# Optimization experiments

Measured on AMD Instinct MI355X. Metric: run time of the kernel, lower is better.

The kernel has to match this reference:

```python
import jax, jax.numpy as jnp
import numpy as np
from jax import lax

# Matches init_kwargs: ops='co', window_size=[51, 25]
OPS = "co"
WINDOWS = [51, 25]


def _stage(x, k, mode):
    # Torch Conv1d(padding='same') zero-pads left=(k-1)//2, right=k//2, and the
    # identity-shift kernel bank + channel min/max is exactly a sliding-window
    # min/max over the zero-padded signal.
    left, right = (k - 1) // 2, k // 2
    xp = jnp.pad(x, ((0, 0), (0, 0), (left, right)))  # zeros, as in torch 'same'
    if mode == "max":  # dilation
        return lax.reduce_window(xp, float("-inf"), lax.max, (1, 1, k), (1, 1, 1), "VALID")
    # erosion
    return lax.reduce_window(xp, float("inf"), lax.min, (1, 1, k), (1, 1, 1), "VALID")


def _chain(x):
    # Per-channel python loop in the original is channel-independent; we batch it.
    for op, k in zip(OPS, WINDOWS):
        if op.lower() == "c":  # closing: dilation then erosion
            x = _stage(x, k, "max")
            x = _stage(x, k, "min")
        elif op.lower() == "o":  # opening: erosion then dilation
            x = _stage(x, k, "min")
            x = _stage(x, k, "max")
    return x


def setup_inputs() -> dict:
    key = jax.random.key(0)
    x = jax.random.normal(key, (16, 8, 262144), dtype=jnp.float32)  # [B, C, L]
    return {"x": x}


def reference(x):
    return _chain(x)
```

## Files before the change

### kernel.cpp

```cpp
#include <hip/hip_runtime.h>


#define L_ROW   262144
#define N_ROWS  128
#define BLOCK   64
#define E       32
#define EF4     8
#define T_W     1880
#define N_CHUNKS 140
#define NSLOT   512

typedef float f32x2 __attribute__((ext_vector_type(2)));

__device__ __forceinline__ int swz(int s) { return s ^ ((s >> 3) & 7); }

#define WFENCE() asm volatile("" ::: "memory")

template<bool MX>
__device__ __forceinline__ float mm(float a, float b) {
  return MX ? fmaxf(a, b) : fminf(a, b);
}

__device__ __forceinline__ void edge_zero(float* r, int goff, int lane, bool edge) {
  if (edge) {
    const int base = goff + lane * E;
#pragma unroll
    for (int i = 0; i < E; ++i)
      if ((unsigned)(base + i) >= (unsigned)L_ROW) r[i] = 0.0f;
  }
}

__device__ __forceinline__ void writeback(const float* r, float4* buf, int b4) {
  WFENCE();
#pragma unroll
  for (int j = 0; j < EF4; ++j)
    buf[swz(b4 + j)] = make_float4(r[4*j], r[4*j+1], r[4*j+2], r[4*j+3]);
  WFENCE();
}

template<int K, bool MX>
__device__ __forceinline__ void stage_big(float* r, float4* buf, int lane,
                                          int goff, bool edge) {
  constexpr int BLEN = K - 33;
  constexpr int BN   = (BLEN + 2) / 4;
  const int b4 = lane * EF4;
  const int bh = min(b4, NSLOT - 16 - BN);

  float4 v0 = buf[swz(bh + 8)];
  float a0 = v0.x, a1 = v0.y, a2 = v0.z, a3 = v0.w;
#pragma unroll
  for (int j = 1; j < BN - 1; ++j) {
    float4 v = buf[swz(bh + 8 + j)];
    a0 = mm<MX>(a0, v.x); a1 = mm<MX>(a1, v.y);
    a2 = mm<MX>(a2, v.z); a3 = mm<MX>(a3, v.w);
  }
  float4 vl = buf[swz(bh + 8 + BN - 1)];
  const float Base = mm<MX>(mm<MX>(mm<MX>(a0, a1), mm<MX>(a2, a3)),
                            mm<MX>(vl.x, vl.y));
  float T[34];
  T[0] = vl.z; T[1] = vl.w;
#pragma unroll
  for (int j = 0; j < 8; ++j) {
    float4 v = buf[swz(bh + 8 + BN + j)];
    T[2+4*j] = v.x; T[3+4*j] = v.y; T[4+4*j] = v.z; T[5+4*j] = v.w;
  }

#pragma unroll
  for (int b = 0; b < 4; ++b)
#pragma unroll
    for (int i = 8*b + 6; i >= 8*b; --i) r[i] = mm<MX>(r[i], r[i+1]);
  const float S2 = r[24];
  const float S1 = mm<MX>(r[16], S2);
  const float S0 = mm<MX>(r[8],  S1);
#pragma unroll
  for (int i = 0;  i < 8;  ++i) r[i] = mm<MX>(r[i], S0);
#pragma unroll
  for (int i = 8;  i < 16; ++i) r[i] = mm<MX>(r[i], S1);
#pragma unroll
  for (int i = 16; i < 24; ++i) r[i] = mm<MX>(r[i], S2);

#pragma unroll
  for (int b = 0; b < 4; ++b)
#pragma unroll
    for (int i = 8*b + 1; i < 8*b + 8; ++i) T[i] = mm<MX>(T[i-1], T[i]);
  const float G0 = mm<MX>(Base, T[7]);
  const float G1 = mm<MX>(G0,   T[15]);
  const float G2 = mm<MX>(G1,   T[23]);

#pragma unroll
  for (int i = 0;  i < 8;  ++i) r[i] = mm<MX>(r[i], mm<MX>(Base, T[i]));
#pragma unroll
  for (int i = 8;  i < 16; ++i) r[i] = mm<MX>(r[i], mm<MX>(G0, T[i]));
#pragma unroll
  for (int i = 16; i < 24; ++i) r[i] = mm<MX>(r[i], mm<MX>(G1, T[i]));
#pragma unroll
  for (int i = 24; i < 32; ++i) r[i] = mm<MX>(r[i], mm<MX>(G2, T[i]));

  edge_zero(r, goff, lane, edge);
  writeback(r, buf, b4);
}

template<bool MX>
__device__ __forceinline__ void stage_25(float* r, float4* buf, int lane,
                                         int goff, bool edge) {
  const int b4 = lane * EF4;
  const int bh = min(b4, NSLOT - 14);
  float h[24];
#pragma unroll
  for (int j = 0; j < 6; ++j) {
    float4 v = buf[swz(bh + 8 + j)];
    h[4*j] = v.x; h[4*j+1] = v.y; h[4*j+2] = v.z; h[4*j+3] = v.w;
  }

  float t[8];
  t[0] = r[24];
#pragma unroll
  for (int i = 1; i < 8; ++i) t[i] = mm<MX>(t[i-1], r[24+i]);
#pragma unroll
  for (int i = 30; i >= 24; --i) r[i] = mm<MX>(r[i], r[i+1]);
#pragma unroll
  for (int i = 22; i >= 16; --i) r[i] = mm<MX>(r[i], r[i+1]);
  const float cA = r[16];
  const float A3 = r[24];
#pragma unroll
  for (int i = 16; i < 24; ++i) r[i] = mm<MX>(r[i], A3);
#pragma unroll
  for (int i = 14; i >= 8; --i) r[i] = mm<MX>(r[i], r[i+1]);
#pragma unroll
  for (int i = 6;  i >= 0; --i) r[i] = mm<MX>(r[i], r[i+1]);
  const float A1 = r[8];
#pragma unroll
  for (int i = 0; i < 8; ++i) r[i] = mm<MX>(r[i], A1);
#pragma unroll
  for (int b = 0; b < 3; ++b)
#pragma unroll
    for (int i = 8*b + 1; i < 8*b + 8; ++i) h[i] = mm<MX>(h[i-1], h[i]);
  const float aB  = h[7];
  const float cA2 = mm<MX>(cA, t[7]);
  const float G1  = mm<MX>(aB, h[15]);
#pragma unroll
  for (int i = 0;  i < 8;  ++i) r[i] = mm<MX>(r[i], mm<MX>(cA,  t[i]));
#pragma unroll
  for (int i = 8;  i < 16; ++i) r[i] = mm<MX>(r[i], mm<MX>(cA2, h[i-8]));
#pragma unroll
  for (int i = 16; i < 24; ++i) r[i] = mm<MX>(r[i], mm<MX>(aB,  h[i-8]));
#pragma unroll
  for (int i = 24; i < 32; ++i) r[i] = mm<MX>(r[i], mm<MX>(G1,  h[i-8]));

  edge_zero(r, goff, lane, edge);
  writeback(r, buf, b4);
}

__global__ __launch_bounds__(BLOCK)
void morph_co_kernel(const float* __restrict__ x, float* __restrict__ out) {
  __shared__ float4 buf[NSLOT];

  const int lane = threadIdx.x;
  const int c    = blockIdx.x;
  const int row  = blockIdx.y;

  const float* __restrict__ xrow = x   + (size_t)row * L_ROW;
  float* __restrict__       orow = out + (size_t)row * L_ROW;

  const int ob = c * T_W;
  const int c0 = ob - 76;
  const bool edge = (c == 0) || (c == N_CHUNKS - 1);
  const int b4 = lane * EF4;

  if (!edge) {
#pragma unroll
    for (int it = 0; it < 8; ++it) {
      const int s = it * 64 + lane;
      const float* g = xrow + c0 + 4 * swz(s);
      __builtin_amdgcn_global_load_lds(
          (const __attribute__((address_space(1))) void*)g,
          (__attribute__((address_space(3))) void*)(&buf[it * 64]), 16, 0, 0);
    }
    asm volatile("s_waitcnt vmcnt(0)" ::: "memory");
  } else {
#pragma unroll
    for (int it = 0; it < 8; ++it) {
      const int s = it * 64 + lane;
      const int g = c0 + 4 * s;
      float4 v;
      v.x = ((unsigned)(g + 0) < (unsigned)L_ROW) ? xrow[g + 0] : 0.0f;
      v.y = ((unsigned)(g + 1) < (unsigned)L_ROW) ? xrow[g + 1] : 0.0f;
      v.z = ((unsigned)(g + 2) < (unsigned)L_ROW) ? xrow[g + 2] : 0.0f;
      v.w = ((unsigned)(g + 3) < (unsigned)L_ROW) ? xrow[g + 3] : 0.0f;
      buf[swz(s)] = v;
    }
    WFENCE();
  }

  float r[E];
#pragma unroll
  for (int j = 0; j < EF4; ++j) {
    float4 v = buf[swz(b4 + j)];
    r[4*j] = v.x; r[4*j+1] = v.y; r[4*j+2] = v.z; r[4*j+3] = v.w;
  }

  if (!edge) {
    stage_big<51, true >(r, buf, lane, 0, false);
    stage_big<75, false>(r, buf, lane, 0, false);
    stage_25 <true >(r, buf, lane, 0, false);
  } else {
    stage_big<51, true >(r, buf, lane, c0 + 25, true);
    stage_big<51, false>(r, buf, lane, c0 + 50, true);
    stage_25 <false>(r, buf, lane, c0 + 62, true);
    stage_25 <true >(r, buf, lane, c0 + 74, true);
  }

  if (!edge) {
#pragma unroll
    for (int it = 0; it < 8; ++it) {
      const int u = it * 64 + lane;
      if (u <= T_W / 4) {
        float4 v = buf[swz(u)];
        float* p = orow + ob + 4 * u;
        if (u >= 1)       *reinterpret_cast<f32x2*>(p - 2) = f32x2{v.x, v.y};
        if (u < T_W / 4)  *reinterpret_cast<f32x2*>(p)     = f32x2{v.z, v.w};
      }
    }
  } else {
    const int hi = min(ob + T_W, L_ROW);
#pragma unroll
    for (int it = 0; it < 8; ++it) {
      const int u = it * 64 + lane;
      if (u <= T_W / 4) {
        float4 v = buf[swz(u)];
        const int p = ob - 2 + 4 * u;
        if (p     >= ob && p     < hi) orow[p]     = v.x;
        if (p + 1 >= ob && p + 1 < hi) orow[p + 1] = v.y;
        if (p + 2 >= ob && p + 2 < hi) orow[p + 2] = v.z;
        if (p + 3 >= ob && p + 3 < hi) orow[p + 3] = v.w;
      }
    }
  }
}

extern "C" void kernel_launch(void* const* d_in, const int* in_sizes, int n_in,
                              void* d_out, int out_size, void* d_ws, size_t ws_size,
                              hipStream_t stream) {
  const float* x = (const float*)d_in[0];
  float* out = (float*)d_out;
  dim3 grid(N_CHUNKS, N_ROWS);
  morph_co_kernel<<<grid, BLOCK, 0, stream>>>(x, out);
}
```

Baseline: 50.47 us.

## Double per-lane element count to 64 and widen chunks to cut halo overhead

Each lane now holds 64 elements instead of 32, and each block covers a tile of about 4000 outputs instead of 1880, with fewer chunks per row. The stage kernels are rewritten as prefix/suffix scans over 64-element registers, and the swizzle is adjusted for the larger LDS buffer. The goal is to cut the redundant halo loads and halo computation per output and to amortize the window scans over more elements. In exchange each lane holds many more registers, which risks lower occupancy, and the grid has fewer blocks (66x128).

```diff
diff --git a/kernel.cpp b/kernel.cpp
--- a/kernel.cpp
+++ b/kernel.cpp
@@ -4,15 +4,14 @@
 #define L_ROW   262144
 #define N_ROWS  128
 #define BLOCK   64
-#define E       32
-#define EF4     8
-#define T_W     1880
-#define N_CHUNKS 140
-#define NSLOT   512
+#define E       64
+#define T_W     3996
+#define N_CHUNKS 66
+#define NSLOT   1048
 
 typedef float f32x2 __attribute__((ext_vector_type(2)));
 
-__device__ __forceinline__ int swz(int s) { return s ^ ((s >> 3) & 7); }
+__device__ __forceinline__ int swz(int s) { return s ^ ((s >> 4) & 7); }
 
 #define WFENCE() asm volatile("" ::: "memory")
 
@@ -21,50 +20,8 @@
   return MX ? fmaxf(a, b) : fminf(a, b);
 }
 
-__device__ __forceinline__ void edge_zero(float* r, int goff, int lane, bool edge) {
-  if (edge) {
-    const int base = goff + lane * E;
-#pragma unroll
-    for (int i = 0; i < E; ++i)
-      if ((unsigned)(base + i) >= (unsigned)L_ROW) r[i] = 0.0f;
-  }
-}
-
-__device__ __forceinline__ void writeback(const float* r, float4* buf, int b4) {
-  WFENCE();
-#pragma unroll
-  for (int j = 0; j < EF4; ++j)
-    buf[swz(b4 + j)] = make_float4(r[4*j], r[4*j+1], r[4*j+2], r[4*j+3]);
-  WFENCE();
-}
-
-template<int K, bool MX>
-__device__ __forceinline__ void stage_big(float* r, float4* buf, int lane,
-                                          int goff, bool edge) {
-  constexpr int BLEN = K - 33;
-  constexpr int BN   = (BLEN + 2) / 4;
-  const int b4 = lane * EF4;
-  const int bh = min(b4, NSLOT - 16 - BN);
-
-  float4 v0 = buf[swz(bh + 8)];
-  float a0 = v0.x, a1 = v0.y, a2 = v0.z, a3 = v0.w;
-#pragma unroll
-  for (int j = 1; j < BN - 1; ++j) {
-    float4 v = buf[swz(bh + 8 + j)];
-    a0 = mm<MX>(a0, v.x); a1 = mm<MX>(a1, v.y);
-    a2 = mm<MX>(a2, v.z); a3 = mm<MX>(a3, v.w);
-  }
-  float4 vl = buf[swz(bh + 8 + BN - 1)];
-  const float Base = mm<MX>(mm<MX>(mm<MX>(a0, a1), mm<MX>(a2, a3)),
-                            mm<MX>(vl.x, vl.y));
-  float T[34];
-  T[0] = vl.z; T[1] = vl.w;
-#pragma unroll
-  for (int j = 0; j < 8; ++j) {
-    float4 v = buf[swz(bh + 8 + BN + j)];
-    T[2+4*j] = v.x; T[3+4*j] = v.y; T[4+4*j] = v.z; T[5+4*j] = v.w;
-  }
-
+template<bool MX>
+__device__ __forceinline__ void suffix32(float* r) {
 #pragma unroll
   for (int b = 0; b < 4; ++b)
 #pragma unroll
@@ -78,77 +35,199 @@
   for (int i = 8;  i < 16; ++i) r[i] = mm<MX>(r[i], S1);
 #pragma unroll
   for (int i = 16; i < 24; ++i) r[i] = mm<MX>(r[i], S2);
-
-#pragma unroll
-  for (int b = 0; b < 4; ++b)
-#pragma unroll
-    for (int i = 8*b + 1; i < 8*b + 8; ++i) T[i] = mm<MX>(T[i-1], T[i]);
-  const float G0 = mm<MX>(Base, T[7]);
-  const float G1 = mm<MX>(G0,   T[15]);
-  const float G2 = mm<MX>(G1,   T[23]);
-
-#pragma unroll
-  for (int i = 0;  i < 8;  ++i) r[i] = mm<MX>(r[i], mm<MX>(Base, T[i]));
-#pragma unroll
-  for (int i = 8;  i < 16; ++i) r[i] = mm<MX>(r[i], mm<MX>(G0, T[i]));
-#pragma unroll
-  for (int i = 16; i < 24; ++i) r[i] = mm<MX>(r[i], mm<MX>(G1, T[i]));
-#pragma unroll
-  for (int i = 24; i < 32; ++i) r[i] = mm<MX>(r[i], mm<MX>(G2, T[i]));
-
-  edge_zero(r, goff, lane, edge);
-  writeback(r, buf, b4);
-}
-
-template<bool MX>
-__device__ __forceinline__ void stage_25(float* r, float4* buf, int lane,
-                                         int goff, bool edge) {
-  const int b4 = lane * EF4;
-  const int bh = min(b4, NSLOT - 14);
+}
+
+template<bool MX>
+__device__ __forceinline__ void suffix16(float* r) {
+#pragma unroll
+  for (int i = 6; i >= 0; --i)  r[i] = mm<MX>(r[i], r[i+1]);
+#pragma unroll
+  for (int i = 14; i >= 8; --i) r[i] = mm<MX>(r[i], r[i+1]);
+  const float S = r[8];
+#pragma unroll
+  for (int i = 0; i < 8; ++i) r[i] = mm<MX>(r[i], S);
+}
+
+template<int NF4>
+__device__ __forceinline__ void read_h(const float4* buf, int base, float* h) {
+#pragma unroll
+  for (int j = 0; j < NF4; ++j) {
+    float4 v = buf[swz(base + j)];
+    h[4*j] = v.x; h[4*j+1] = v.y; h[4*j+2] = v.z; h[4*j+3] = v.w;
+  }
+}
+
+template<int N, bool MX>
+__device__ __forceinline__ void prefix_blocks(float* h) {
+#pragma unroll
+  for (int b = 0; b < N/8; ++b)
+#pragma unroll
+    for (int i = 8*b + 1; i < 8*b + 8; ++i) h[i] = mm<MX>(h[i-1], h[i]);
+}
+
+template<int N, bool MX>
+__device__ __forceinline__ void cascade(float* h) {
+#pragma unroll
+  for (int b = 1; b < N/8; ++b) {
+    const float cc = h[8*b - 1];
+#pragma unroll
+    for (int i = 8*b; i < 8*b + 8; ++i) h[i] = mm<MX>(cc, h[i]);
+  }
+}
+
+template<int N, bool MX>
+__device__ __forceinline__ void cascade_from(float* h, float carry) {
+  float cc = carry;
+#pragma unroll
+  for (int b = 0; b < N/8; ++b) {
+#pragma unroll
+    for (int i = 8*b; i < 8*b + 8; ++i) h[i] = mm<MX>(cc, h[i]);
+    cc = h[8*b + 7];
+  }
+}
+
+__device__ __forceinline__ void edge_zero64(float* r, int goff, int lane, bool edge) {
+  if (edge) {
+    const int base = goff + lane * E;
+#pragma unroll
+    for (int i = 0; i < E; ++i)
+      if ((unsigned)(base + i) >= (unsigned)L_ROW) r[i] = 0.0f;
+  }
+}
+
+__device__ __forceinline__ void writeback(const float* r, float4* buf, int b16) {
+  WFENCE();
+#pragma unroll
+  for (int j = 0; j < 16; ++j)
+    buf[swz(b16 + j)] = make_float4(r[4*j], r[4*j+1], r[4*j+2], r[4*j+3]);
+  WFENCE();
+}
+
+template<bool MX>
+__device__ __forceinline__ void stage51(float* r, float4* buf, int lane,
+                                        int goff, bool edge) {
+  const int hb = lane * 16 + 16;
+  float tp[14];
+  float c = r[32];
+#pragma unroll
+  for (int j = 1; j < 32; ++j) {
+    c = mm<MX>(c, r[32 + j]);
+    if (j >= 18) tp[j - 18] = c;
+  }
+  const float RA = c;
+  float h[20];
+  read_h<5>(buf, hb, h);
+  prefix_blocks<16, MX>(h);
+#pragma unroll
+  for (int i = 17; i < 20; ++i) h[i] = mm<MX>(h[i-1], h[i]);
+  { const float cc = h[7];
+#pragma unroll
+    for (int i = 8; i < 16; ++i) h[i] = mm<MX>(cc, h[i]); }
+  { const float cc = h[15];
+#pragma unroll
+    for (int i = 16; i < 20; ++i) h[i] = mm<MX>(cc, h[i]); }
+  const float s18 = h[18], s19 = h[19];
+
+  suffix32<MX>(r);
+#pragma unroll
+  for (int i = 0; i < 14; ++i)  r[i] = mm<MX>(r[i], tp[i]);
+#pragma unroll
+  for (int i = 14; i < 32; ++i) r[i] = mm<MX>(r[i], mm<MX>(RA, h[i-14]));
+
+  float h2[32];
+  read_h<8>(buf, hb + 5, h2);
+  prefix_blocks<32, MX>(h2);
+  cascade_from<32, MX>(h2, s19);
+
+  suffix32<MX>(r + 32);
+  r[32] = mm<MX>(r[32], s18);
+  r[33] = mm<MX>(r[33], s19);
+#pragma unroll
+  for (int i = 34; i < 64; ++i) r[i] = mm<MX>(r[i], h2[i-34]);
+
+  edge_zero64(r, goff, lane, edge);
+  writeback(r, buf, lane * 16);
+}
+
+template<bool MX>
+__device__ __forceinline__ void stage75(float* r, float4* buf, int lane,
+                                        int goff, bool edge) {
+  const int hb = lane * 16 + 16;
+  float c = r[32];
+#pragma unroll
+  for (int j = 1; j < 32; ++j) c = mm<MX>(c, r[32 + j]);
+  const float RA = c;
+  float h[44];
+  read_h<11>(buf, hb, h);
+  prefix_blocks<40, MX>(h);
+#pragma unroll
+  for (int i = 41; i < 44; ++i) h[i] = mm<MX>(h[i-1], h[i]);
+  cascade<40, MX>(h);
+  { const float cc = h[39];
+#pragma unroll
+    for (int i = 40; i < 44; ++i) h[i] = mm<MX>(cc, h[i]); }
+  const float c42 = h[42], c43 = h[43];
+
+  suffix32<MX>(r);
+#pragma unroll
+  for (int i = 0; i < 32; ++i) r[i] = mm<MX>(r[i], mm<MX>(RA, h[i+10]));
+
+  float h2[32];
+  read_h<8>(buf, hb + 11, h2);
+  prefix_blocks<32, MX>(h2);
+  cascade_from<32, MX>(h2, c43);
+
+  suffix32<MX>(r + 32);
+  r[32] = mm<MX>(r[32], c42);
+  r[33] = mm<MX>(r[33], c43);
+#pragma unroll
+  for (int i = 34; i < 64; ++i) r[i] = mm<MX>(r[i], h2[i-34]);
+
+  edge_zero64(r, goff, lane, edge);
+  writeback(r, buf, lane * 16);
+}
+
+template<bool MX>
+__device__ __forceinline__ void stage25(float* r, float4* buf, int lane,
+                                        int goff, bool edge) {
+  const int hb = lane * 16 + 16;
   float h[24];
-#pragma unroll
-  for (int j = 0; j < 6; ++j) {
-    float4 v = buf[swz(bh + 8 + j)];
-    h[4*j] = v.x; h[4*j+1] = v.y; h[4*j+2] = v.z; h[4*j+3] = v.w;
-  }
-
-  float t[8];
-  t[0] = r[24];
-#pragma unroll
-  for (int i = 1; i < 8; ++i) t[i] = mm<MX>(t[i-1], r[24+i]);
-#pragma unroll
-  for (int i = 30; i >= 24; --i) r[i] = mm<MX>(r[i], r[i+1]);
-#pragma unroll
-  for (int i = 22; i >= 16; --i) r[i] = mm<MX>(r[i], r[i+1]);
-  const float cA = r[16];
-  const float A3 = r[24];
-#pragma unroll
-  for (int i = 16; i < 24; ++i) r[i] = mm<MX>(r[i], A3);
-#pragma unroll
-  for (int i = 14; i >= 8; --i) r[i] = mm<MX>(r[i], r[i+1]);
-#pragma unroll
-  for (int i = 6;  i >= 0; --i) r[i] = mm<MX>(r[i], r[i+1]);
-  const float A1 = r[8];
-#pragma unroll
-  for (int i = 0; i < 8; ++i) r[i] = mm<MX>(r[i], A1);
-#pragma unroll
-  for (int b = 0; b < 3; ++b)
-#pragma unroll
-    for (int i = 8*b + 1; i < 8*b + 8; ++i) h[i] = mm<MX>(h[i-1], h[i]);
-  const float aB  = h[7];
-  const float cA2 = mm<MX>(cA, t[7]);
-  const float G1  = mm<MX>(aB, h[15]);
-#pragma unroll
-  for (int i = 0;  i < 8;  ++i) r[i] = mm<MX>(r[i], mm<MX>(cA,  t[i]));
-#pragma unroll
-  for (int i = 8;  i < 16; ++i) r[i] = mm<MX>(r[i], mm<MX>(cA2, h[i-8]));
-#pragma unroll
-  for (int i = 16; i < 24; ++i) r[i] = mm<MX>(r[i], mm<MX>(aB,  h[i-8]));
-#pragma unroll
-  for (int i = 24; i < 32; ++i) r[i] = mm<MX>(r[i], mm<MX>(G1,  h[i-8]));
-
-  edge_zero(r, goff, lane, edge);
-  writeback(r, buf, b4);
+  read_h<6>(buf, hb, h);
+
+  float p2[16];
+  { float c = r[48];
+#pragma unroll
+    for (int j = 1; j < 16; ++j) { c = mm<MX>(c, r[48+j]); if (j >= 8) p2[j-8] = c; }
+#pragma unroll
+    for (int j = 0; j < 8; ++j)  { c = mm<MX>(c, h[j]); p2[8+j] = c; } }
+  float p1[16];
+  { float c = r[32];
+#pragma unroll
+    for (int j = 1; j < 24; ++j) { c = mm<MX>(c, r[32+j]); if (j >= 8) p1[j-8] = c; } }
+  prefix_blocks<24, MX>(h);
+  cascade<24, MX>(h);
+
+  suffix16<MX>(r + 48);
+#pragma unroll
+  for (int i = 48; i < 64; ++i) r[i] = mm<MX>(r[i], h[i-40]);
+
+  float p0[16];
+  { float c = r[16];
+#pragma unroll
+    for (int j = 1; j < 24; ++j) { c = mm<MX>(c, r[16+j]); if (j >= 8) p0[j-8] = c; } }
+
+  suffix16<MX>(r + 32);
+#pragma unroll
+  for (int i = 32; i < 48; ++i) r[i] = mm<MX>(r[i], p2[i-32]);
+  suffix16<MX>(r + 16);
+#pragma unroll
+  for (int i = 16; i < 32; ++i) r[i] = mm<MX>(r[i], p1[i-16]);
+  suffix16<MX>(r);
+#pragma unroll
+  for (int i = 0; i < 16; ++i)  r[i] = mm<MX>(r[i], p0[i]);
+
+  edge_zero64(r, goff, lane, edge);
+  writeback(r, buf, lane * 16);
 }
 
 __global__ __launch_bounds__(BLOCK)
@@ -165,54 +244,65 @@
   const int ob = c * T_W;
   const int c0 = ob - 76;
   const bool edge = (c == 0) || (c == N_CHUNKS - 1);
-  const int b4 = lane * EF4;
 
   if (!edge) {
 #pragma unroll
-    for (int it = 0; it < 8; ++it) {
+    for (int it = 0; it < 16; ++it) {
       const int s = it * 64 + lane;
       const float* g = xrow + c0 + 4 * swz(s);
       __builtin_amdgcn_global_load_lds(
           (const __attribute__((address_space(1))) void*)g,
           (__attribute__((address_space(3))) void*)(&buf[it * 64]), 16, 0, 0);
     }
+    if (lane < NSLOT - 1024) {
+      const int s = 1024 + lane;
+      const float* g = xrow + c0 + 4 * swz(s);
+      __builtin_amdgcn_global_load_lds(
+          (const __attribute__((address_space(1))) void*)g,
+          (__attribute__((address_space(3))) void*)(&buf[1024]), 16, 0, 0);
+    }
     asm volatile("s_waitcnt vmcnt(0)" ::: "memory");
   } else {
 #pragma unroll
-    for (int it = 0; it < 8; ++it) {
+    for (int it = 0; it < 17; ++it) {
       const int s = it * 64 + lane;
-      const int g = c0 + 4 * s;
-      float4 v;
-      v.x = ((unsigned)(g + 0) < (unsigned)L_ROW) ? xrow[g + 0] : 0.0f;
-      v.y = ((unsigned)(g + 1) < (unsigned)L_ROW) ? xrow[g + 1] : 0.0f;
-      v.z = ((unsigned)(g + 2) < (unsigned)L_ROW) ? xrow[g + 2] : 0.0f;
-      v.w = ((unsigned)(g + 3) < (unsigned)L_ROW) ? xrow[g + 3] : 0.0f;
-      buf[swz(s)] = v;
+      if (s < NSLOT) {
+        const int g = c0 + 4 * s;
+        float4 v;
+        v.x = ((unsigned)(g + 0) < (unsigned)L_ROW) ? xrow[g + 0] : 0.0f;
+        v.y = ((unsigned)(g + 1) < (unsigned)L_ROW) ? xrow[g + 1] : 0.0f;
+        v.z = ((unsigned)(g + 2) < (unsigned)L_ROW) ? xrow[g + 2] : 0.0f;
+        v.w = ((unsigned)(g + 3) < (unsigned)L_ROW) ? xrow[g + 3] : 0.0f;
+        buf[swz(s)] = v;
+      }
     }
     WFENCE();
   }
 
   float r[E];
-#pragma unroll
-  for (int j = 0; j < EF4; ++j) {
-    float4 v = buf[swz(b4 + j)];
-    r[4*j] = v.x; r[4*j+1] = v.y; r[4*j+2] = v.z; r[4*j+3] = v.w;
+  {
+    const int b16 = lane * 16;
+#pragma unroll
+    for (int j = 0; j < 16; ++j) {
+      float4 v = buf[swz(b16 + j)];
+      r[4*j] = v.x; r[4*j+1] = v.y; r[4*j+2] = v.z; r[4*j+3] = v.w;
+    }
   }
 
   if (!edge) {
-    stage_big<51, true >(r, buf, lane, 0, false);
-    stage_big<75, false>(r, buf, lane, 0, false);
-    stage_25 <true >(r, buf, lane, 0, false);
+    stage51<true >(r, buf, lane, 0, false);
+    stage75<false>(r, buf, lane, 0, false);
+    stage25<true >(r, buf, lane, 0, false);
   } else {
-    stage_big<51, true >(r, buf, lane, c0 + 25, true);
-    stage_big<51, false>(r, buf, lane, c0 + 50, true);
-    stage_25 <false>(r, buf, lane, c0 + 62, true);
-    stage_25 <true >(r, buf, lane, c0 + 74, true);
+    stage51<true >(r, buf, lane, c0 + 25, true);
+    stage51<false>(r, buf, lane, c0 + 50, true);
+    stage25<false>(r, buf, lane, c0 + 62, true);
+    stage25<true >(r, buf, lane, c0 + 74, true);
   }
 
   if (!edge) {
 #pragma unroll
-    for (int it = 0; it < 8; ++it) {
+    for (int it = 0; it < 16; ++it) {
       const int u = it * 64 + lane;
       if (u <= T_W / 4) {
         float4 v = buf[swz(u)];
@@ -224,7 +314,7 @@
   } else {
     const int hi = min(ob + T_W, L_ROW);
 #pragma unroll
-    for (int it = 0; it < 8; ++it) {
+    for (int it = 0; it < 16; ++it) {
       const int u = it * 64 + lane;
       if (u <= T_W / 4) {
         float4 v = buf[swz(u)];
```

New measurement: 69.75 us. 38.2% more time.
